# Optimization experiments

Measured on AMD Instinct MI355X. Metric: run time of the kernel, lower is better.

The kernel has to match this reference:

```python
import jax, jax.numpy as jnp
import numpy as np

NUM_HEADS = 16
HEAD_DIM = 64
HIDDEN = 1024
ROPE_BASE = 10000.0


def _rope_cache(seq_len, dtype):
    inv_freq = 1.0 / (ROPE_BASE ** (jnp.arange(0, HEAD_DIM, 2, dtype=jnp.float32) / HEAD_DIM))
    freqs = jnp.arange(seq_len, dtype=jnp.float32)[:, None] * inv_freq[None, :]  # [S, D/2]
    emb = jnp.concatenate([freqs, freqs], axis=-1)  # [S, D]
    return jnp.cos(emb).astype(dtype), jnp.sin(emb).astype(dtype)


def _rotate_half(x):
    x1, x2 = jnp.split(x, 2, axis=-1)
    return jnp.concatenate([-x2, x1], axis=-1)


def setup_inputs() -> dict:
    key = jax.random.key(0)
    k1, k2, k3 = jax.random.split(key, 3)
    B, S = 1, 4096
    x = jax.random.normal(k1, (B, S, HIDDEN), dtype=jnp.float32)
    w_qkv = jax.random.normal(k2, (3 * HIDDEN, HIDDEN), dtype=jnp.float32) * (1.0 / np.sqrt(HIDDEN))
    w_out = jax.random.normal(k3, (HIDDEN, HIDDEN), dtype=jnp.float32) * (1.0 / np.sqrt(HIDDEN))
    return {"x": x, "w_qkv": w_qkv, "w_out": w_out}


def reference(x, w_qkv, w_out):
    B, S, _ = x.shape
    scale = 1.0 / np.sqrt(HEAD_DIM)
    # fused QKV projection (torch Linear: x @ W^T)
    qkv = jnp.einsum('bsd,ed->bse', x, w_qkv)
    qkv = qkv.reshape(B, S, 3, NUM_HEADS, HEAD_DIM).transpose(2, 0, 3, 1, 4)
    q, k, v = qkv[0], qkv[1], qkv[2]  # [B, H, S, Dh]
    cos, sin = _rope_cache(S, x.dtype)  # [S, Dh]
    cos = cos[None, None]
    sin = sin[None, None]
    q = q * cos + _rotate_half(q) * sin
    k = k * cos + _rotate_half(k) * sin
    scores = jnp.einsum('bhqd,bhkd->bhqk', q, k) * scale  # [B, H, S, S]
    causal = jnp.triu(jnp.ones((S, S), dtype=bool), k=1)
    min_val = jnp.finfo(scores.dtype).min
    scores = jnp.where(causal[None, None], min_val, scores)
    attn = jax.nn.softmax(scores, axis=-1)
    out = jnp.einsum('bhqk,bhkd->bhqd', attn, v)  # [B, H, S, Dh]
    out = out.transpose(0, 2, 1, 3).reshape(B, S, HIDDEN)
    return jnp.einsum('bsd,ed->bse', out, w_out)
```

## Files before the change

### kernel.cpp

```cpp
#include <hip/hip_runtime.h>

#define S_LEN 4096
#define NHEAD 16
#define DHEAD 64
#define HID 1024

typedef float f32x4 __attribute__((ext_vector_type(4)));
typedef float f32x16 __attribute__((ext_vector_type(16)));
typedef unsigned short u16x8 __attribute__((ext_vector_type(8)));
typedef __bf16 bf16x8 __attribute__((ext_vector_type(8)));

__device__ __forceinline__ unsigned short f2bf(float f) {
  union { float f; unsigned u; } x; x.f = f;
  return (unsigned short)((x.u + 0x7FFFu + ((x.u >> 16) & 1u)) >> 16);
}
__device__ __forceinline__ float bf2f(unsigned short u) {
  union { unsigned u; float f; } x; x.u = ((unsigned)u) << 16;
  return x.f;
}
__device__ __forceinline__ f32x4 mfma16(u16x8 a, u16x8 b, f32x4 c) {
  return __builtin_amdgcn_mfma_f32_16x16x32_bf16(
      __builtin_bit_cast(bf16x8, a), __builtin_bit_cast(bf16x8, b), c, 0, 0, 0);
}
__device__ __forceinline__ f32x16 mfma32(u16x8 a, u16x8 b, f32x16 c) {
  return __builtin_amdgcn_mfma_f32_32x32x16_bf16(
      __builtin_bit_cast(bf16x8, a), __builtin_bit_cast(bf16x8, b), c, 0, 0, 0);
}
__device__ __forceinline__ void gload16(const void* g, void* l) {
  __builtin_amdgcn_global_load_lds(
      (const __attribute__((address_space(1))) void*)g,
      (__attribute__((address_space(3))) void*)l, 16, 0, 0);
}
__device__ __forceinline__ void permswap(unsigned& a, unsigned& b) {
#if __has_builtin(__builtin_amdgcn_permlane32_swap)
  typedef unsigned u32x2 __attribute__((ext_vector_type(2)));
  u32x2 r = __builtin_amdgcn_permlane32_swap(a, b, false, false);
  a = r[0]; b = r[1];
#else
  asm volatile("v_permlane32_swap_b32 %0, %1" : "+v"(a), "+v"(b));
#endif
}
__device__ __forceinline__ unsigned cvtpk(float lo, float hi) {
  unsigned r;
  asm("v_cvt_pk_bf16_f32 %0, %1, %2" : "=v"(r) : "v"(lo), "v"(hi));
  return r;
}
__device__ __forceinline__ float fexp2(float x) {
  float r;
  asm("v_exp_f32 %0, %1" : "=v"(r) : "v"(x));
  return r;
}

__global__ void k_cvt_all(const float4* __restrict__ x, const float4* __restrict__ wq,
                          const float4* __restrict__ wo, ushort4* __restrict__ xb,
                          ushort4* __restrict__ wqb, ushort4* __restrict__ wob) {
  int i = blockIdx.x * blockDim.x + threadIdx.x;
  const float4* src; ushort4* dst; int off;
  if (i < 1048576)      { src = x;  dst = xb;  off = i; }
  else if (i < 1835008) { src = wq; dst = wqb; off = i - 1048576; }
  else                  { src = wo; dst = wob; off = i - 1835008; }
  float4 v = src[off];
  ushort4 o;
  o.x = f2bf(v.x); o.y = f2bf(v.y); o.z = f2bf(v.z); o.w = f2bf(v.w);
  dst[off] = o;
}

__global__ void k_rope_split(const unsigned short* __restrict__ qkv,
                             unsigned short* __restrict__ Q,
                             unsigned short* __restrict__ Kf) {
  int s = blockIdx.x;
  int t = threadIdx.x;
  int h = t >> 5, i = t & 31;
  float inv = fexp2(-(float)i * 0.4152410118609203f);
  float ang = (float)s * inv;
  float sn, cs;
  __sincosf(ang, &sn, &cs);
  const unsigned short* row = qkv + (size_t)s * 3072;
  float q1 = bf2f(row[h * 64 + i]);
  float q2 = bf2f(row[h * 64 + i + 32]);
  float k1 = bf2f(row[1024 + h * 64 + i]);
  float k2 = bf2f(row[1024 + h * 64 + i + 32]);
  const float ksc = 0.125f * 1.44269504f;
  size_t qo = ((size_t)h * S_LEN + s) * 64 + i;
  Q[qo]      = f2bf(q1 * cs - q2 * sn);
  Q[qo + 32] = f2bf(q2 * cs + q1 * sn);
  int t32 = s >> 5, kv = s & 31;
  size_t ko = ((((size_t)h * 128 + t32) * 4 + (i >> 4)) * 2 + ((i >> 3) & 1)) * 256 + kv * 8 + (i & 7);
  Kf[ko]        = f2bf((k1 * cs - k2 * sn) * ksc);
  Kf[ko + 1024] = f2bf((k2 * cs + k1 * sn) * ksc);
}

__global__ void k_vt(const unsigned short* __restrict__ qkv,
                     unsigned short* __restrict__ Vf) {
  __shared__ unsigned short tile[64][65];
  int st = blockIdx.x, h = blockIdx.y;
  int t = threadIdx.x;
  int r = t >> 2, c0 = (t & 3) * 16;
  const unsigned short* src = qkv + (size_t)(st * 64 + r) * 3072 + 2048 + h * 64 + c0;
  u16x8 a = *(const u16x8*)src;
  u16x8 b = *(const u16x8*)(src + 8);
#pragma unroll
  for (int j = 0; j < 8; ++j) { tile[r][c0 + j] = a[j]; tile[r][c0 + 8 + j] = b[j]; }
  __syncthreads();
#pragma unroll
  for (int pass = 0; pass < 2; ++pass) {
    int task = t + pass * 256;
    int o = task >> 6, d = task & 63;
    int t32 = st * 2 + (o >> 2), kc = (o >> 1) & 1, hfv = o & 1;
    u16x8 v;
#pragma unroll
    for (int e = 0; e < 8; ++e) v[e] = tile[o * 8 + e][d];
    *(u16x8*)(Vf + (((((size_t)h * 128 + t32) * 2 + kc) * 2 + hfv) * 64 + d) * 8) = v;
  }
}

__device__ __forceinline__ void stc(float* p, float v) { *p = v; }
__device__ __forceinline__ void stc(unsigned short* p, float v) { *p = f2bf(v); }

template <typename OutT>
__global__ __launch_bounds__(256, 3) void gemm_bt(
    const unsigned short* __restrict__ A, const unsigned short* __restrict__ B,
    OutT* __restrict__ C, int M, int N, int K) {
  __shared__ __attribute__((aligned(16))) unsigned short As[3][128][32];
  __shared__ __attribute__((aligned(16))) unsigned short Bs[3][128][32];
  const int tid = threadIdx.x;
  const int w = tid >> 6, lane = tid & 63;
  const int bm = blockIdx.y * 128, bn = blockIdx.x * 128;
  const int wr = w >> 1, wc = w & 1;
  const int l16 = lane >> 2;
  const int c4s = ((lane & 3) ^ ((lane >> 3) & 3)) * 8;
  f32x4 acc[4][4] = {};

  auto stage = [&](int buf, int kt) {
    const int k0 = kt << 5;
#pragma unroll
    for (int c = 0; c < 2; ++c) {
      int row = w * 32 + c * 16;
      gload16(A + (size_t)(bm + row + l16) * K + k0 + c4s, &As[buf][row][0]);
      gload16(B + (size_t)(bn + row + l16) * K + k0 + c4s, &Bs[buf][row][0]);
    }
  };

  const int nk = K >> 5;
  stage(0, 0);
  stage(1, 1);
  int cur = 0;
  for (int kt = 0; kt < nk; ++kt) {
    asm volatile("s_waitcnt vmcnt(4)" ::: "memory");
    __builtin_amdgcn_sched_barrier(0);
    __builtin_amdgcn_s_barrier();
    __builtin_amdgcn_sched_barrier(0);
    {
      const int sbuf = (cur + 2 >= 3) ? cur - 1 : cur + 2;
      const int stile = (kt + 2 < nk) ? kt + 2 : nk - 1;
      stage(sbuf, stile);
    }
    const int sph = (((lane >> 4) ^ (lane >> 1)) & 3) * 16;
    u16x8 af[4], bfr[4];
#pragma unroll
    for (int m = 0; m < 4; ++m) {
      int row = wr * 64 + m * 16 + (lane & 15);
      af[m] = *(const u16x8*)((const char*)&As[cur][0][0] + row * 64 + sph);
    }
#pragma unroll
    for (int n = 0; n < 4; ++n) {
      int row = wc * 64 + n * 16 + (lane & 15);
      bfr[n] = *(const u16x8*)((const char*)&Bs[cur][0][0] + row * 64 + sph);
    }
#pragma unroll
    for (int m = 0; m < 4; ++m)
#pragma unroll
      for (int n = 0; n < 4; ++n)
        acc[m][n] = mfma16(af[m], bfr[n], acc[m][n]);
    cur = (cur + 1 == 3) ? 0 : cur + 1;
  }
#pragma unroll
  for (int m = 0; m < 4; ++m) {
    int row = bm + wr * 64 + m * 16 + (lane >> 4) * 4;
#pragma unroll
    for (int n = 0; n < 4; ++n) {
      int col = bn + wc * 64 + n * 16 + (lane & 15);
#pragma unroll
      for (int j = 0; j < 4; ++j) stc(&C[(size_t)(row + j) * N + col], acc[m][n][j]);
    }
  }
}

__device__ __forceinline__ void attn_range(
    const unsigned short* __restrict__ kfb, const unsigned short* __restrict__ vfb,
    const u16x8* qf, f32x16& accA, f32x16& accB, float& l_own,
    int t0, int t1, int nst, int qg, int hf, int kOffBase, int vOffBase) {
  if (t0 >= t1) return;
  u16x8 ka[4], kb_[4], kc2[4], va[4], vb_[4], vc2[4];
#define LOADK(dst, t)                                                         \
  {                                                                           \
    const unsigned short* p_ = kfb + (size_t)(t) * 2048 + kOffBase;           \
    dst[0] = *(const u16x8*)(p_);                                             \
    dst[1] = *(const u16x8*)(p_ + 512);                                       \
    dst[2] = *(const u16x8*)(p_ + 1024);                                      \
    dst[3] = *(const u16x8*)(p_ + 1536);                                      \
  }
#define LOADV(dst, t)                                                         \
  {                                                                           \
    const unsigned short* p_ = vfb + (size_t)(t) * 2048 + vOffBase;           \
    dst[0] = *(const u16x8*)(p_);                                             \
    dst[1] = *(const u16x8*)(p_ + 256);                                       \
    dst[2] = *(const u16x8*)(p_ + 1024);                                      \
    dst[3] = *(const u16x8*)(p_ + 1280);                                      \
  }
#define STEP(t, kc_, vc_, kn_, vn_)                                           \
  {                                                                           \
    const int tn = ((t) + 2 < t1) ? (t) + 2 : t1 - 1;                         \
    LOADK(kn_, tn);                                                           \
    LOADV(vn_, tn);                                                           \
    f32x16 sc = {};                                                           \
    __builtin_amdgcn_s_setprio(1);                                            \
    _Pragma("unroll") for (int c = 0; c < 4; ++c) sc = mfma32(kc_[c], qf[c], sc); \
    __builtin_amdgcn_s_setprio(0);                                            \
    if ((t) == nst - 1) {                     \
      _Pragma("unroll") for (int rr = 0; rr < 16; ++rr) {                     \
        int kvl = (t) * 32 + (rr & 3) + 8 * (rr >> 2) + 4 * hf;               \
        if (kvl > qg) sc[rr] = -1e30f;                                        \
      }                                                                       \
    }                                                                         \
    float p[16];                                                              \
    _Pragma("unroll") for (int rr = 0; rr < 16; ++rr) p[rr] = fexp2(sc[rr]);  \
    l_own += (((p[0] + p[1]) + (p[2] + p[3])) + ((p[4] + p[5]) + (p[6] + p[7]))) + \
             (((p[8] + p[9]) + (p[10] + p[11])) + ((p[12] + p[13]) + (p[14] + p[15]))); \
    unsigned dw[8];                                                           \
    _Pragma("unroll") for (int k = 0; k < 8; ++k) dw[k] = cvtpk(p[2 * k], p[2 * k + 1]); \
    __builtin_amdgcn_s_setprio(1);                                            \
    _Pragma("unroll") for (int kc = 0; kc < 2; ++kc) {                        \
      unsigned x0 = dw[4 * kc + 0], x1 = dw[4 * kc + 1];                      \
      unsigned y0 = dw[4 * kc + 2], y1 = dw[4 * kc + 3];                      \
      permswap(x0, y0);                                                       \
      permswap(x1, y1);                                                       \
      union { u16x8 v; unsigned u[4]; } pf;                                   \
      pf.u[0] = x0; pf.u[1] = x1; pf.u[2] = y0; pf.u[3] = y1;                 \
      accA = mfma32(vc_[kc * 2 + 0], pf.v, accA);                             \
      accB = mfma32(vc_[kc * 2 + 1], pf.v, accB);                             \
    }                                                                         \
    __builtin_amdgcn_s_setprio(0);                                            \
  }

  LOADK(ka, t0);
  LOADV(va, t0);
  {
    const int t1c = (t0 + 1 < t1) ? t0 + 1 : t1 - 1;
    LOADK(kb_, t1c);
    LOADV(vb_, t1c);
  }
  int t = t0;
  while (true) {
    STEP(t, ka, va, kc2, vc2);
    if (++t >= t1) break;
    STEP(t, kb_, vb_, ka, va);
    if (++t >= t1) break;
    STEP(t, kc2, vc2, kb_, vb_);
    if (++t >= t1) break;
  }
#undef STEP
#undef LOADK
#undef LOADV
}

__device__ __forceinline__ void attn_epilogue(
    const f32x16& accA, const f32x16& accB, float l_own, char* eb,
    unsigned short* __restrict__ O, int h, int qb, int wr, int q31, int hf) {
  float l_run;
  {
    unsigned a = __float_as_uint(l_own), b = a;
    permswap(a, b);
    l_run = __uint_as_float(a) + __uint_as_float(b);
  }
  const float inv = 1.0f / l_run;
#pragma unroll
  for (int dblk = 0; dblk < 2; ++dblk) {
#pragma unroll
    for (int tt = 0; tt < 4; ++tt) {
      float a0, a1, a2, a3;
      if (dblk == 0) { a0 = accA[4 * tt]; a1 = accA[4 * tt + 1]; a2 = accA[4 * tt + 2]; a3 = accA[4 * tt + 3]; }
      else           { a0 = accB[4 * tt]; a1 = accB[4 * tt + 1]; a2 = accB[4 * tt + 2]; a3 = accB[4 * tt + 3]; }
      unsigned d0 = cvtpk(a0 * inv, a1 * inv);
      unsigned d1 = cvtpk(a2 * inv, a3 * inv);
      int dbase = dblk * 32 + 8 * tt + 4 * hf;
      int off = (q31 * 128 + dbase * 2) ^ ((q31 & 7) << 4);
      *(uint2*)(eb + off) = make_uint2(d0, d1);
    }
  }
  const int lane = hf * 32 + q31;
#pragma unroll
  for (int pass = 0; pass < 4; ++pass) {
    int q = (lane >> 3) + pass * 8;
    int c8 = lane & 7;
    u16x8 vv = *(const u16x8*)(eb + ((q * 128 + c8 * 16) ^ ((q & 7) << 4)));
    *(u16x8*)(O + (size_t)(qb + wr * 32 + q) * HID + h * 64 + c8 * 8) = vv;
  }
}

__global__ __launch_bounds__(512) void flash_attn(
    const unsigned short* __restrict__ Q,
    const unsigned short* __restrict__ Kf,
    const unsigned short* __restrict__ Vf,
    unsigned short* __restrict__ O) {
  __shared__ __attribute__((aligned(16))) unsigned short ebuf[4][2048];
  __shared__ float part[4][64][34];
  const int tid = threadIdx.x;
  const int wv = tid >> 6, lane = tid & 63;
  const int wr = wv & 3, role = wv >> 2;
  const int q31 = lane & 31, hf = lane >> 5;
  const int h = blockIdx.x;
  const int y = blockIdx.y;
  const int qt = (y < 16) ? (31 - y) : (y - 16);
  const int nst = 4 * qt + wr + 1;
  const int cut = (nst + 1) >> 1;

  const unsigned short* kfb = Kf + (size_t)h * 128 * 2048;
  const unsigned short* vfb = Vf + (size_t)h * 128 * 2048;
  const int kOffBase = hf * 256 + q31 * 8;
  const int vOffBase = hf * 512 + q31 * 8;

  const int qg = qt * 128 + wr * 32 + q31;
  u16x8 qf[4];
  {
    const unsigned short* qp = Q + ((size_t)h * S_LEN + qg) * 64 + hf * 8;
#pragma unroll
    for (int c = 0; c < 4; ++c) qf[c] = *(const u16x8*)(qp + c * 16);
  }

  f32x16 aA = {}, aB = {};
  float al = 0.f;
  if (role == 0) {
    attn_range(kfb, vfb, qf, aA, aB, al, 0, cut, nst, qg, hf, kOffBase, vOffBase);
    float* pp = &part[wr][lane][0];
#pragma unroll
    for (int r = 0; r < 16; ++r) { pp[r] = aA[r]; pp[16 + r] = aB[r]; }
    pp[32] = al;
    __syncthreads();
  } else {
    attn_range(kfb, vfb, qf, aA, aB, al, cut, nst, nst, qg, hf, kOffBase, vOffBase);
    __syncthreads();
    const float* pp = &part[wr][lane][0];
#pragma unroll
    for (int r = 0; r < 16; ++r) { aA[r] += pp[r]; aB[r] += pp[16 + r]; }
    al += pp[32];
    attn_epilogue(aA, aB, al, (char*)&ebuf[wr][0], O, h, qt * 128, wr, q31, hf);
  }
}

extern "C" void kernel_launch(void* const* d_in, const int* in_sizes, int n_in,
                              void* d_out, int out_size, void* d_ws, size_t ws_size,
                              hipStream_t stream) {
  const float* x = (const float*)d_in[0];
  const float* w_qkv = (const float*)d_in[1];
  const float* w_out = (const float*)d_in[2];
  float* out = (float*)d_out;
  char* ws = (char*)d_ws;

  unsigned short* xb    = (unsigned short*)(ws + 0);
  unsigned short* wqkvb = (unsigned short*)(ws + 8388608);
  unsigned short* woutb = (unsigned short*)(ws + 14680064);
  unsigned short* qkvb  = (unsigned short*)(ws + 16777216);
  unsigned short* Qb    = (unsigned short*)(ws + 41943040);
  unsigned short* Kfb   = (unsigned short*)(ws + 50331648);
  unsigned short* Vfb   = (unsigned short*)(ws + 58720256);
  unsigned short* attnb = (unsigned short*)(ws + 67108864);

  k_cvt_all<<<dim3(8192), dim3(256), 0, stream>>>(
      (const float4*)x, (const float4*)w_qkv, (const float4*)w_out,
      (ushort4*)xb, (ushort4*)wqkvb, (ushort4*)woutb);

  gemm_bt<unsigned short><<<dim3(24, 32), dim3(256), 0, stream>>>(xb, wqkvb, qkvb, 4096, 3072, 1024);

  k_rope_split<<<dim3(4096), dim3(512), 0, stream>>>(qkvb, Qb, Kfb);
  k_vt<<<dim3(64, 16), dim3(256), 0, stream>>>(qkvb, Vfb);

  flash_attn<<<dim3(16, 32), dim3(512), 0, stream>>>(Qb, Kfb, Vfb, attnb);

  gemm_bt<float><<<dim3(8, 32), dim3(256), 0, stream>>>(attnb, woutb, out, 4096, 1024, 1024);
}
```

Baseline: 140.4 us.

## Pair causal query tiles per block and stage K/V through shared LDS ring

Each attention block now handles two query tiles, a short one and its mirror long one, so every block does a balanced amount of causal work. The grid is halved. K/V tiles are loaded cooperatively with async global-to-LDS loads into a triple-buffered ring, and all warps read their fragments from LDS instead of each warp loading from global memory on its own. This cuts redundant global K/V traffic across the four query-row warps. The cost is a block-wide barrier every round, more LDS use that may lower occupancy, and a serial split-combine step between the two tiles.

Measured after the change: 141.8 us. Within noise of the previous version (+1.0%).

```diff
diff --git a/kernel.cpp b/kernel.cpp
--- a/kernel.cpp
+++ b/kernel.cpp
@@ -186,84 +186,6 @@
   }
 }
 
-__device__ __forceinline__ void attn_range(
-    const unsigned short* __restrict__ kfb, const unsigned short* __restrict__ vfb,
-    const u16x8* qf, f32x16& accA, f32x16& accB, float& l_own,
-    int t0, int t1, int nst, int qg, int hf, int kOffBase, int vOffBase) {
-  if (t0 >= t1) return;
-  u16x8 ka[4], kb_[4], kc2[4], va[4], vb_[4], vc2[4];
-#define LOADK(dst, t)                                                         \
-  {                                                                           \
-    const unsigned short* p_ = kfb + (size_t)(t) * 2048 + kOffBase;           \
-    dst[0] = *(const u16x8*)(p_);                                             \
-    dst[1] = *(const u16x8*)(p_ + 512);                                       \
-    dst[2] = *(const u16x8*)(p_ + 1024);                                      \
-    dst[3] = *(const u16x8*)(p_ + 1536);                                      \
-  }
-#define LOADV(dst, t)                                                         \
-  {                                                                           \
-    const unsigned short* p_ = vfb + (size_t)(t) * 2048 + vOffBase;           \
-    dst[0] = *(const u16x8*)(p_);                                             \
-    dst[1] = *(const u16x8*)(p_ + 256);                                       \
-    dst[2] = *(const u16x8*)(p_ + 1024);                                      \
-    dst[3] = *(const u16x8*)(p_ + 1280);                                      \
-  }
-#define STEP(t, kc_, vc_, kn_, vn_)                                           \
-  {                                                                           \
-    const int tn = ((t) + 2 < t1) ? (t) + 2 : t1 - 1;                         \
-    LOADK(kn_, tn);                                                           \
-    LOADV(vn_, tn);                                                           \
-    f32x16 sc = {};                                                           \
-    __builtin_amdgcn_s_setprio(1);                                            \
-    _Pragma("unroll") for (int c = 0; c < 4; ++c) sc = mfma32(kc_[c], qf[c], sc); \
-    __builtin_amdgcn_s_setprio(0);                                            \
-    if ((t) == nst - 1) {                     \
-      _Pragma("unroll") for (int rr = 0; rr < 16; ++rr) {                     \
-        int kvl = (t) * 32 + (rr & 3) + 8 * (rr >> 2) + 4 * hf;               \
-        if (kvl > qg) sc[rr] = -1e30f;                                        \
-      }                                                                       \
-    }                                                                         \
-    float p[16];                                                              \
-    _Pragma("unroll") for (int rr = 0; rr < 16; ++rr) p[rr] = fexp2(sc[rr]);  \
-    l_own += (((p[0] + p[1]) + (p[2] + p[3])) + ((p[4] + p[5]) + (p[6] + p[7]))) + \
-             (((p[8] + p[9]) + (p[10] + p[11])) + ((p[12] + p[13]) + (p[14] + p[15]))); \
-    unsigned dw[8];                                                           \
-    _Pragma("unroll") for (int k = 0; k < 8; ++k) dw[k] = cvtpk(p[2 * k], p[2 * k + 1]); \
-    __builtin_amdgcn_s_setprio(1);                                            \
-    _Pragma("unroll") for (int kc = 0; kc < 2; ++kc) {                        \
-      unsigned x0 = dw[4 * kc + 0], x1 = dw[4 * kc + 1];                      \
-      unsigned y0 = dw[4 * kc + 2], y1 = dw[4 * kc + 3];                      \
-      permswap(x0, y0);                                                       \
-      permswap(x1, y1);                                                       \
-      union { u16x8 v; unsigned u[4]; } pf;                                   \
-      pf.u[0] = x0; pf.u[1] = x1; pf.u[2] = y0; pf.u[3] = y1;                 \
-      accA = mfma32(vc_[kc * 2 + 0], pf.v, accA);                             \
-      accB = mfma32(vc_[kc * 2 + 1], pf.v, accB);                             \
-    }                                                                         \
-    __builtin_amdgcn_s_setprio(0);                                            \
-  }
-
-  LOADK(ka, t0);
-  LOADV(va, t0);
-  {
-    const int t1c = (t0 + 1 < t1) ? t0 + 1 : t1 - 1;
-    LOADK(kb_, t1c);
-    LOADV(vb_, t1c);
-  }
-  int t = t0;
-  while (true) {
-    STEP(t, ka, va, kc2, vc2);
-    if (++t >= t1) break;
-    STEP(t, kb_, vb_, ka, va);
-    if (++t >= t1) break;
-    STEP(t, kc2, vc2, kb_, vb_);
-    if (++t >= t1) break;
-  }
-#undef STEP
-#undef LOADK
-#undef LOADV
-}
-
 __device__ __forceinline__ void attn_epilogue(
     const f32x16& accA, const f32x16& accB, float l_own, char* eb,
     unsigned short* __restrict__ O, int h, int qb, int wr, int q31, int hf) {
@@ -303,49 +225,147 @@
     const unsigned short* __restrict__ Kf,
     const unsigned short* __restrict__ Vf,
     unsigned short* __restrict__ O) {
+  __shared__ __attribute__((aligned(16))) unsigned short kv_lds[3][2][4096];
+  __shared__ float part[4][64][34];
   __shared__ __attribute__((aligned(16))) unsigned short ebuf[4][2048];
-  __shared__ float part[4][64][34];
   const int tid = threadIdx.x;
   const int wv = tid >> 6, lane = tid & 63;
   const int wr = wv & 3, role = wv >> 2;
   const int q31 = lane & 31, hf = lane >> 5;
   const int h = blockIdx.x;
-  const int y = blockIdx.y;
-  const int qt = (y < 16) ? (31 - y) : (y - 16);
-  const int nst = 4 * qt + wr + 1;
-  const int cut = (nst + 1) >> 1;
+  const int p = blockIdx.y;
+  const int tileB = 31 - p;
+  const int nA = 4 * p + 4;
+  const int rA = nA >> 1;
+  const int nstA = 4 * p + wr + 1;
+  const int nstB = 4 * tileB + wr + 1;
+  const int NR = 66;
 
   const unsigned short* kfb = Kf + (size_t)h * 128 * 2048;
   const unsigned short* vfb = Vf + (size_t)h * 128 * 2048;
-  const int kOffBase = hf * 256 + q31 * 8;
-  const int vOffBase = hf * 512 + q31 * 8;
-
-  const int qg = qt * 128 + wr * 32 + q31;
-  u16x8 qf[4];
+
+  auto stageRound = [&](int buf, int r) {
+#pragma unroll
+    for (int k = 0; k < 2; ++k) {
+      int g = 2 * r + k;
+      if (g > 131) g = 131;
+      const int kvt = (g < nA) ? g : g - nA;
+      const unsigned short* src =
+          ((tid >= 256) ? vfb : kfb) + (size_t)kvt * 2048 + (size_t)(tid & 255) * 8;
+      char* dst = (char*)&kv_lds[buf][k][0] + (tid >> 8) * 4096 + (tid & 255) * 16;
+      gload16(src, dst);
+    }
+  };
+
+  u16x8 qfA[4], qfB[4];
   {
-    const unsigned short* qp = Q + ((size_t)h * S_LEN + qg) * 64 + hf * 8;
-#pragma unroll
-    for (int c = 0; c < 4; ++c) qf[c] = *(const u16x8*)(qp + c * 16);
-  }
+    const unsigned short* qa = Q + ((size_t)h * S_LEN + p * 128 + wr * 32 + q31) * 64 + hf * 8;
+    const unsigned short* qb2 = Q + ((size_t)h * S_LEN + tileB * 128 + wr * 32 + q31) * 64 + hf * 8;
+#pragma unroll
+    for (int c = 0; c < 4; ++c) { qfA[c] = *(const u16x8*)(qa + c * 16); qfB[c] = *(const u16x8*)(qb2 + c * 16); }
+  }
+
+  stageRound(0, 0);
+  stageRound(1, 1);
 
   f32x16 aA = {}, aB = {};
   float al = 0.f;
+
+#define KSTEP(r_, kvt_, qf_, qg_, nst_, xA, xB, xl)                            \
+  {                                                                            \
+    const char* tb = (const char*)&kv_lds[(r_) % 3][role][0];                  \
+    if ((kvt_) < (nst_)) {                                                     \
+      u16x8 kfr[4], vfr[4];                                                    \
+      _Pragma("unroll") for (int c = 0; c < 4; ++c)                            \
+        kfr[c] = *(const u16x8*)(tb + c * 1024 + hf * 512 + q31 * 16);         \
+      _Pragma("unroll") for (int kc = 0; kc < 2; ++kc)                         \
+        _Pragma("unroll") for (int j = 0; j < 2; ++j)                          \
+          vfr[kc * 2 + j] = *(const u16x8*)(tb + 4096 + kc * 2048 + hf * 1024 + (q31 + 32 * j) * 16); \
+      f32x16 sc = {};                                                          \
+      __builtin_amdgcn_s_setprio(1);                                           \
+      _Pragma("unroll") for (int c = 0; c < 4; ++c) sc = mfma32(kfr[c], qf_[c], sc); \
+      __builtin_amdgcn_s_setprio(0);                                           \
+      if ((kvt_) == (nst_) - 1) {                                              \
+        _Pragma("unroll") for (int rr = 0; rr < 16; ++rr) {                    \
+          int kvl = (kvt_) * 32 + (rr & 3) + 8 * (rr >> 2) + 4 * hf;           \
+          if (kvl > (qg_)) sc[rr] = -1e30f;                                    \
+        }                                                                      \
+      }                                                                        \
+      float pe[16];                                                            \
+      _Pragma("unroll") for (int rr = 0; rr < 16; ++rr) pe[rr] = fexp2(sc[rr]); \
+      xl += (((pe[0] + pe[1]) + (pe[2] + pe[3])) + ((pe[4] + pe[5]) + (pe[6] + pe[7]))) + \
+            (((pe[8] + pe[9]) + (pe[10] + pe[11])) + ((pe[12] + pe[13]) + (pe[14] + pe[15]))); \
+      unsigned dw[8];                                                          \
+      _Pragma("unroll") for (int k = 0; k < 8; ++k) dw[k] = cvtpk(pe[2 * k], pe[2 * k + 1]); \
+      __builtin_amdgcn_s_setprio(1);                                           \
+      _Pragma("unroll") for (int kc = 0; kc < 2; ++kc) {                       \
+        unsigned x0 = dw[4 * kc + 0], x1 = dw[4 * kc + 1];                     \
+        unsigned y0 = dw[4 * kc + 2], y1 = dw[4 * kc + 3];                     \
+        permswap(x0, y0);                                                      \
+        permswap(x1, y1);                                                      \
+        union { u16x8 v; unsigned u[4]; } pf;                                  \
+        pf.u[0] = x0; pf.u[1] = x1; pf.u[2] = y0; pf.u[3] = y1;                \
+        xA = mfma32(vfr[kc * 2 + 0], pf.v, xA);                                \
+        xB = mfma32(vfr[kc * 2 + 1], pf.v, xB);                                \
+      }                                                                        \
+      __builtin_amdgcn_s_setprio(0);                                           \
+    }                                                                          \
+  }
+
+#define ROUND_SYNC(r_)                                                         \
+  asm volatile("s_waitcnt vmcnt(2)" ::: "memory");                             \
+  __builtin_amdgcn_sched_barrier(0);                                           \
+  __builtin_amdgcn_s_barrier();                                                \
+  __builtin_amdgcn_sched_barrier(0);                                           \
+  stageRound(((r_) + 2) % 3, (r_) + 2);
+
+  const int qgA = p * 128 + wr * 32 + q31;
+  for (int r = 0; r < rA; ++r) {
+    ROUND_SYNC(r);
+    const int kvt = 2 * r + role;
+    KSTEP(r, kvt, qfA, qgA, nstA, aA, aB, al);
+  }
+  if (role == 1) {
+    float* pp = &part[wr][lane][0];
+#pragma unroll
+    for (int r2 = 0; r2 < 16; ++r2) { pp[r2] = aA[r2]; pp[16 + r2] = aB[r2]; }
+    pp[32] = al;
+  }
+  asm volatile("s_waitcnt lgkmcnt(0)" ::: "memory");
+  __builtin_amdgcn_s_barrier();
   if (role == 0) {
-    attn_range(kfb, vfb, qf, aA, aB, al, 0, cut, nst, qg, hf, kOffBase, vOffBase);
+    const float* pp = &part[wr][lane][0];
+#pragma unroll
+    for (int r2 = 0; r2 < 16; ++r2) { aA[r2] += pp[r2]; aB[r2] += pp[16 + r2]; }
+    al += pp[32];
+    attn_epilogue(aA, aB, al, (char*)&ebuf[wr][0], O, h, p * 128, wr, q31, hf);
+  }
+
+  f32x16 bA = {}, bB = {};
+  float bl = 0.f;
+  const int qgB = tileB * 128 + wr * 32 + q31;
+  for (int r = rA; r < NR; ++r) {
+    ROUND_SYNC(r);
+    const int kvt = 2 * r + role - nA;
+    KSTEP(r, kvt, qfB, qgB, nstB, bA, bB, bl);
+  }
+  if (role == 0) {
     float* pp = &part[wr][lane][0];
 #pragma unroll
-    for (int r = 0; r < 16; ++r) { pp[r] = aA[r]; pp[16 + r] = aB[r]; }
-    pp[32] = al;
-    __syncthreads();
-  } else {
-    attn_range(kfb, vfb, qf, aA, aB, al, cut, nst, nst, qg, hf, kOffBase, vOffBase);
-    __syncthreads();
+    for (int r2 = 0; r2 < 16; ++r2) { pp[r2] = bA[r2]; pp[16 + r2] = bB[r2]; }
+    pp[32] = bl;
+  }
+  asm volatile("s_waitcnt lgkmcnt(0)" ::: "memory");
+  __builtin_amdgcn_s_barrier();
+  if (role == 1) {
     const float* pp = &part[wr][lane][0];
 #pragma unroll
-    for (int r = 0; r < 16; ++r) { aA[r] += pp[r]; aB[r] += pp[16 + r]; }
-    al += pp[32];
-    attn_epilogue(aA, aB, al, (char*)&ebuf[wr][0], O, h, qt * 128, wr, q31, hf);
-  }
+    for (int r2 = 0; r2 < 16; ++r2) { bA[r2] += pp[r2]; bB[r2] += pp[16 + r2]; }
+    bl += pp[32];
+    attn_epilogue(bA, bB, bl, (char*)&ebuf[wr][0], O, h, tileB * 128, wr, q31, hf);
+  }
+#undef KSTEP
+#undef ROUND_SYNC
 }
 
 extern "C" void kernel_launch(void* const* d_in, const int* in_sizes, int n_in,
@@ -375,7 +395,7 @@
   k_rope_split<<<dim3(4096), dim3(512), 0, stream>>>(qkvb, Qb, Kfb);
   k_vt<<<dim3(64, 16), dim3(256), 0, stream>>>(qkvb, Vfb);
 
-  flash_attn<<<dim3(16, 32), dim3(512), 0, stream>>>(Qb, Kfb, Vfb, attnb);
+  flash_attn<<<dim3(16, 16), dim3(512), 0, stream>>>(Qb, Kfb, Vfb, attnb);
 
   gemm_bt<float><<<dim3(8, 32), dim3(256), 0, stream>>>(attnb, woutb, out, 4096, 1024, 1024);
 }
```
